# Kernel optimization log

Hardware: AMD Instinct MI355X
Metric: run time of the kernel (lower is better)

Reference implementation:

```python
import jax, jax.numpy as jnp
import numpy as np

VAR0, VAR1 = 0.1, 0.2          # SSD encode variances
POS_T, NEG_T, NPR = 0.5, 0.4, 3  # pos/neg thresholds, negpos_ratio
BBOX_ALPHA, CONF_ALPHA = 1.5, 1.0


def point_form(b):
    # cxcywh -> x1y1x2y2
    return jnp.concatenate([b[..., :2] - b[..., 2:] / 2, b[..., :2] + b[..., 2:] / 2], -1)


def jaccard(a, b):
    # a:[n,4], b:[m,4] in xyxy -> IoU [n,m]
    tl = jnp.maximum(a[:, None, :2], b[None, :, :2])
    br = jnp.minimum(a[:, None, 2:], b[None, :, 2:])
    inter = jnp.prod(jnp.clip(br - tl, 0.0), -1)
    area_a = jnp.prod(a[:, 2:] - a[:, :2], -1)[:, None]
    area_b = jnp.prod(b[:, 2:] - b[:, :2], -1)[None, :]
    return inter / jnp.clip(area_a + area_b - inter, 1e-10)


def encode(matched, priors):
    # matched: xyxy GT per prior; priors: cxcywh
    g_c = ((matched[:, :2] + matched[:, 2:]) / 2 - priors[:, :2]) / (VAR0 * priors[:, 2:])
    g_wh = jnp.log(jnp.clip((matched[:, 2:] - matched[:, :2]) / priors[:, 2:], 1e-8)) / VAR1
    return jnp.concatenate([g_c, g_wh], -1)


def match_one(gt_box, gt_lab, priors):
    # gt_box:[G,4] xyxy, gt_lab:[G], priors:[P,4] cxcywh
    ov = jaccard(gt_box, point_form(priors))            # [G,P]
    bt_over = ov.max(0)                                  # best GT overlap per prior [P]
    bt_idx = ov.argmax(0)                                # [P]
    bp_idx = ov.argmax(1)                                # best prior per GT [G]
    G = gt_box.shape[0]
    bt_over = bt_over.at[bp_idx].set(2.0)                # force-match best priors
    bt_idx = bt_idx.at[bp_idx].set(jnp.arange(G))
    matched = gt_box[bt_idx]                             # [P,4]
    conf_t = gt_lab[bt_idx]
    conf_t = jnp.where(bt_over < POS_T, jnp.where(bt_over < NEG_T, 0, -1), conf_t)
    return encode(matched, priors), conf_t


def reference(loc_data, conf_data, priors, gt_bboxes, gt_labels):
    B, P, C = conf_data.shape
    loc_t, conf_t = jax.vmap(match_one)(gt_bboxes, gt_labels, priors)
    loc_t = jax.lax.stop_gradient(loc_t)                 # targets are detached in torch
    pos = conf_t > 0                                     # [B,P]
    num_pos = pos.sum(-1)                                # [B]
    dt = loc_data.dtype
    pos_w = pos.astype(dt) / jnp.clip(num_pos, 1).astype(dt)[:, None]

    # localization: per-image-normalized smooth L1 over positives
    d = loc_data - loc_t
    sl1 = jnp.where(jnp.abs(d) < 1.0, 0.5 * d * d, jnp.abs(d) - 0.5)
    loss_B = (pos_w[:, :, None] * sl1).sum() * BBOX_ALPHA

    # OHEM confidence loss: mine top negpos_ratio*num_pos hardest negatives per image
    loss_c = jax.nn.logsumexp(conf_data, -1) - conf_data[..., 0]
    loss_c = jnp.where(pos | (conf_t < 0), 0.0, jax.lax.stop_gradient(loss_c))
    rank = jnp.argsort(jnp.argsort(-loss_c, -1), -1)     # descending rank [B,P]
    num_neg = jnp.clip(NPR * num_pos, 0, P - 1)
    neg = (rank < num_neg[:, None]) & (conf_t == 0)
    keep = (pos | neg).astype(dt)
    logp = jax.nn.log_softmax(conf_data, -1)
    tgt = jnp.clip(conf_t, 0)
    ce = -jnp.take_along_axis(logp, tgt[..., None], -1)[..., 0]
    loss_C = (keep * ce).sum() * CONF_ALPHA

    return jnp.stack([loss_B, loss_C]) / B               # [2]: (loss_B, loss_C)


def setup_inputs() -> dict:
    key = jax.random.key(0)
    k = jax.random.split(key, 8)
    B, P, C, G = 16, 19248, 81, 16
    loc_data = jax.random.normal(k[0], (B, P, 4), jnp.float32)
    conf_data = jax.random.normal(k[1], (B, P, C), jnp.float32)
    pc = jax.random.uniform(k[2], (B, P, 2)) * 0.9 + 0.05
    pwh = jax.random.uniform(k[3], (B, P, 2)) * 0.25 + 0.05
    priors = jnp.concatenate([pc, pwh], -1).astype(jnp.float32)  # cxcywh
    gc = jax.random.uniform(k[4], (B, G, 2)) * 0.8 + 0.1
    gwh = jax.random.uniform(k[5], (B, G, 2)) * 0.3 + 0.05
    gt_bboxes = jnp.clip(point_form(jnp.concatenate([gc, gwh], -1)), 0.0, 1.0).astype(jnp.float32)
    gt_labels = jax.random.randint(k[6], (B, G), 1, C)
    return {"loc_data": loc_data, "conf_data": conf_data, "priors": priors,
            "gt_bboxes": gt_bboxes, "gt_labels": gt_labels}
```

## Files before the change

### kernel.cpp

```cpp
#include <hip/hip_runtime.h>
#include <math.h>

#define NB 16
#define NP 19248
#define NC 81
#define NG 16
#define NBM 76
#define NBC 301
#define NWPB (NBC * 4)

static __device__ __forceinline__ float smoothl1(float d) {
    float a = fabsf(d);
    return (a < 1.f) ? 0.5f * d * d : (a - 0.5f);
}

static __device__ __forceinline__ unsigned long long umax64(unsigned long long a, unsigned long long b) {
    return a > b ? a : b;
}

__global__ void k_init(unsigned int* w, float* out) {
    if (threadIdx.x < 512) w[threadIdx.x] = 0u;
    if (threadIdx.x < 2) out[threadIdx.x] = 0.f;
}

__global__ void k_match(const float* __restrict__ priors,
                        const float* __restrict__ gtb,
                        unsigned long long* __restrict__ bp_key) {
    const int b = blockIdx.y;
    const int p = blockIdx.x * 256 + threadIdx.x;
    const bool valid = p < NP;
    __shared__ float4 sgt[NG];
    __shared__ unsigned long long smax[NG];
    if (threadIdx.x < NG) {
        const float* g4 = gtb + (size_t)(b * NG + threadIdx.x) * 4;
        sgt[threadIdx.x] = make_float4(g4[0], g4[1], g4[2], g4[3]);
        smax[threadIdx.x] = 0ULL;
    }
    __syncthreads();
    float4 pr = make_float4(0.f, 0.f, 0.f, 0.f);
    if (valid) pr = *(const float4*)(priors + ((size_t)b * NP + p) * 4);
    const float px1 = pr.x - pr.z * 0.5f, py1 = pr.y - pr.w * 0.5f;
    const float px2 = pr.x + pr.z * 0.5f, py2 = pr.y + pr.w * 0.5f;
    const float areaP = (px2 - px1) * (py2 - py1);
    const unsigned int pk = 0xFFFFFFFFu - (unsigned int)p;
    #pragma unroll
    for (int g = 0; g < NG; ++g) {
        float4 gb = sgt[g];
        float iw = fminf(gb.z, px2) - fmaxf(gb.x, px1);
        float ih = fminf(gb.w, py2) - fmaxf(gb.y, py1);
        float inter = fmaxf(iw, 0.f) * fmaxf(ih, 0.f);
        float areaG = (gb.z - gb.x) * (gb.w - gb.y);
        float ov = inter / fmaxf(areaG + areaP - inter, 1e-10f);
        unsigned long long key = ((unsigned long long)__float_as_uint(ov) << 32) | pk;
        #pragma unroll
        for (int off = 1; off <= 8; off <<= 1)
            key = umax64(key, (unsigned long long)__shfl_xor((unsigned long long)key, off));
        if ((threadIdx.x & 15) == 0) atomicMax(&smax[g], key);
    }
    __syncthreads();
    if (threadIdx.x < NG) atomicMax(&bp_key[b * NG + threadIdx.x], smax[threadIdx.x]);
}

__global__ void __launch_bounds__(256, 6) k_conf(
        const float* __restrict__ conf,
        const float* __restrict__ loc,
        const float* __restrict__ priors,
        const float* __restrict__ gtb,
        const int* __restrict__ gtl,
        const unsigned long long* __restrict__ bp_key,
        float* __restrict__ mlc,
        int* __restrict__ pnp, float* __restrict__ psl, float* __restrict__ pce) {
    __shared__ float sc[4][1296];
    const int b = blockIdx.y;
    const int tid = threadIdx.x;
    const int w = tid >> 6, lane = tid & 63;
    const int rb = blockIdx.x * 64 + w * 16;
    const bool wvalid = rb < NP;
    const int rb_c = wvalid ? rb : (NP - 16);

    const float4* src = (const float4*)(conf + ((size_t)b * NP + rb_c) * 81);
    float4* dst = (float4*)sc[w];
    #pragma unroll
    for (int i = 0; i < 5; ++i) dst[lane + 64 * i] = src[lane + 64 * i];
    if (lane < 4) dst[lane + 320] = src[lane + 320];

    const int r = lane >> 2, c = lane & 3;
    const int p = rb_c + r;
    const int bp = b * NP + p;

    const float4 prr = *(const float4*)(priors + (size_t)bp * 4);
    const float px1 = prr.x - prr.z * 0.5f, py1 = prr.y - prr.w * 0.5f;
    const float px2 = prr.x + prr.z * 0.5f, py2 = prr.y + prr.w * 0.5f;
    const float areaP = (px2 - px1) * (py2 - py1);
    unsigned long long kq = 0ULL;
    #pragma unroll
    for (int j = 0; j < 4; ++j) {
        const int g = c * 4 + j;
        const float* g4 = gtb + (size_t)(b * NG + g) * 4;
        float gx1 = g4[0], gy1 = g4[1], gx2 = g4[2], gy2 = g4[3];
        float iw = fminf(gx2, px2) - fmaxf(gx1, px1);
        float ih = fminf(gy2, py2) - fmaxf(gy1, py1);
        float inter = fmaxf(iw, 0.f) * fmaxf(ih, 0.f);
        float areaG = (gx2 - gx1) * (gy2 - gy1);
        float ov = inter / fmaxf(areaG + areaP - inter, 1e-10f);
        kq = umax64(kq, ((unsigned long long)__float_as_uint(ov) << 32) |
                        (unsigned long long)(15 - g));
    }
    kq = umax64(kq, (unsigned long long)__shfl_xor((unsigned long long)kq, 1, 4));
    kq = umax64(kq, (unsigned long long)__shfl_xor((unsigned long long)kq, 2, 4));
    const float over = __uint_as_float((unsigned int)(kq >> 32));
    int bi = 15 - (int)(kq & 0xFULL);

    int ct;
    if (over < 0.4f) ct = 0;
    else if (over < 0.5f) ct = -1;
    else ct = gtl[b * NG + bi];
    #pragma unroll
    for (int g = NG - 1; g >= 0; --g) {
        unsigned int fp = 0xFFFFFFFFu - (unsigned int)(bp_key[b * NG + g] & 0xFFFFFFFFULL);
        if (fp == (unsigned int)p) { bi = g; ct = gtl[b * NG + g]; break; }
    }
    if (!wvalid) ct = 0;
    const int tgt = ct > 0 ? ct : 0;

    __builtin_amdgcn_wave_barrier();

    const float* row = sc[w] + r * 81;
    float s = 0.f, ctg = 0.f;
    #pragma unroll
    for (int k = 0; k < 21; ++k) {
        int cc = c + 4 * k;
        if (cc < 81) {
            float v = row[cc];
            s += __expf(v);
            ctg += (cc == tgt) ? v : 0.f;
        }
    }
    s += __shfl_xor(s, 1, 4);   s += __shfl_xor(s, 2, 4);
    ctg += __shfl_xor(ctg, 1, 4); ctg += __shfl_xor(ctg, 2, 4);
    const float c0 = row[0];
    const float lse = __logf(s);

    if (c == 0 && wvalid) mlc[bp] = (ct == 0) ? (lse - c0) : -1.0f;

    float vsl = 0.f, vce = 0.f; int vnp = 0;
    if (c == 0 && ct > 0) {
        const float* gb = gtb + (size_t)(b * NG + bi) * 4;
        float lt0 = ((gb[0] + gb[2]) * 0.5f - prr.x) / (0.1f * prr.z);
        float lt1 = ((gb[1] + gb[3]) * 0.5f - prr.y) / (0.1f * prr.w);
        float lt2 = logf(fmaxf((gb[2] - gb[0]) / prr.z, 1e-8f)) / 0.2f;
        float lt3 = logf(fmaxf((gb[3] - gb[1]) / prr.w, 1e-8f)) / 0.2f;
        const float4 l4 = *(const float4*)(loc + (size_t)bp * 4);
        vsl = smoothl1(l4.x - lt0) + smoothl1(l4.y - lt1) +
              smoothl1(l4.z - lt2) + smoothl1(l4.w - lt3);
        vce = lse - ctg;
        vnp = 1;
    }
    #pragma unroll
    for (int o = 32; o >= 1; o >>= 1) {
        vnp += __shfl_xor(vnp, o);
        vsl += __shfl_xor(vsl, o);
        vce += __shfl_xor(vce, o);
    }
    if (lane == 0) {
        const int idx = b * NWPB + blockIdx.x * 4 + w;
        pnp[idx] = vnp; psl[idx] = vsl; pce[idx] = vce;
    }
}

__global__ void __launch_bounds__(1024) k_selneg(
        const float* __restrict__ mlc,
        const int* __restrict__ pnp,
        const float* __restrict__ psl,
        const float* __restrict__ pce,
        float* __restrict__ out) {
    const int b = blockIdx.x, tid = threadIdx.x;
    __shared__ unsigned int hist[4096];
    __shared__ unsigned long long list[1024];
    __shared__ unsigned int s_jstar, s_need, s_cnt;
    __shared__ unsigned long long s_thr;
    __shared__ unsigned int wtot[16], wsuf[16];
    __shared__ float wsum[16];
    __shared__ int wnp[16]; __shared__ float wsl[16], wcp[16];
    __shared__ int s_np; __shared__ float s_sl, s_cp;

    const float4* v4 = (const float4*)(mlc + (size_t)b * NP);
    float4 rv[5];
    #pragma unroll
    for (int j = 0; j < 5; ++j) {
        int i = tid + 1024 * j;
        rv[j] = (i < NP / 4) ? v4[i] : make_float4(-1.f, -1.f, -1.f, -1.f);
    }

    {
        int np_ = 0; float sl_ = 0.f, cp_ = 0.f;
        for (int i = tid; i < NWPB; i += 1024) {
            np_ += pnp[b * NWPB + i];
            sl_ += psl[b * NWPB + i];
            cp_ += pce[b * NWPB + i];
        }
        #pragma unroll
        for (int o = 32; o >= 1; o >>= 1) {
            np_ += __shfl_xor(np_, o);
            sl_ += __shfl_xor(sl_, o);
            cp_ += __shfl_xor(cp_, o);
        }
        if ((tid & 63) == 0) { wnp[tid >> 6] = np_; wsl[tid >> 6] = sl_; wcp[tid >> 6] = cp_; }
    }
    if (tid == 0) { s_cnt = 0u; s_thr = ~0ULL; }
    for (int i = tid; i < 4096; i += 1024) hist[i] = 0u;
    __syncthreads();
    if (tid == 0) {
        int np_ = 0; float sl_ = 0.f, cp_ = 0.f;
        #pragma unroll
        for (int i = 0; i < 16; ++i) { np_ += wnp[i]; sl_ += wsl[i]; cp_ += wcp[i]; }
        s_np = np_; s_sl = sl_; s_cp = cp_;
    }
    #pragma unroll
    for (int j = 0; j < 5; ++j) {
        float vv[4] = {rv[j].x, rv[j].y, rv[j].z, rv[j].w};
        #pragma unroll
        for (int c = 0; c < 4; ++c)
            if (vv[c] >= 0.f)
                atomicAdd(&hist[min((unsigned int)(vv[c] * 256.f), 4095u)], 1u);
    }
    __syncthreads();
    const int np = s_np;
    const unsigned int k = (unsigned int)min(3 * np, NP - 1);

    if (k > 0) {
        unsigned int c0 = hist[tid * 4], c1 = hist[tid * 4 + 1],
                     c2 = hist[tid * 4 + 2], c3 = hist[tid * 4 + 3];
        unsigned int t2 = c2 + c3, t1 = c1 + t2, t0 = c0 + t1;
        unsigned int s = t0;
        const int lane = tid & 63, w = tid >> 6;
        #pragma unroll
        for (int o = 1; o < 64; o <<= 1) {
            unsigned int vv = __shfl_down(s, o);
            if (lane + o < 64) s += vv;
        }
        if (lane == 0) wtot[w] = s;
        __syncthreads();
        if (tid < 16) {
            unsigned int acc = 0;
            for (int j = tid + 1; j < 16; ++j) acc += wtot[j];
            wsuf[tid] = acc;
        }
        __syncthreads();
        const unsigned int base = wsuf[w] + (s - t0);
        unsigned int b0 = base + t0, b1 = base + t1, b2 = base + t2, b3 = base + c3;
        hist[tid * 4] = b0; hist[tid * 4 + 1] = b1;
        hist[tid * 4 + 2] = b2; hist[tid * 4 + 3] = b3;
        __syncthreads();
        const unsigned int total = hist[0];
        if (k >= total) {
            if (tid == 0) s_thr = 0ULL;
        } else {
            unsigned int n3 = (tid * 4 + 4 < 4096) ? hist[tid * 4 + 4] : 0u;
            if (b0 >= k && b1 < k) { s_jstar = tid * 4;     s_need = k - b1; }
            if (b1 >= k && b2 < k) { s_jstar = tid * 4 + 1; s_need = k - b2; }
            if (b2 >= k && b3 < k) { s_jstar = tid * 4 + 2; s_need = k - b3; }
            if (b3 >= k && n3 < k) { s_jstar = tid * 4 + 3; s_need = k - n3; }
            __syncthreads();
            const unsigned int jstar = s_jstar, need = s_need;
            #pragma unroll
            for (int j = 0; j < 5; ++j) {
                float vv[4] = {rv[j].x, rv[j].y, rv[j].z, rv[j].w};
                #pragma unroll
                for (int c = 0; c < 4; ++c) {
                    if (vv[c] >= 0.f &&
                        min((unsigned int)(vv[c] * 256.f), 4095u) == jstar) {
                        unsigned int pos = atomicAdd(&s_cnt, 1u);
                        if (pos < 1024u) {
                            int pidx = 4 * (tid + 1024 * j) + c;
                            list[pos] = ((unsigned long long)__float_as_uint(vv[c]) << 32) |
                                        (unsigned long long)(0xFFFFFFFFu - (unsigned int)pidx);
                        }
                    }
                }
            }
            __syncthreads();
            const unsigned int cnt = s_cnt;
            if (cnt <= 1024u) {
                if (tid < (int)cnt) {
                    unsigned long long me = list[tid];
                    unsigned int rk = 0;
                    for (unsigned int j = 0; j < cnt; ++j) rk += (list[j] > me) ? 1u : 0u;
                    if (rk == need - 1) s_thr = me;
                }
            } else if (tid == 0) {
                s_thr = ((unsigned long long)__float_as_uint((float)jstar / 256.f)) << 32;
            }
        }
    }
    __syncthreads();
    const unsigned long long thr = s_thr;

    float sum = 0.f;
    #pragma unroll
    for (int j = 0; j < 5; ++j) {
        float vv[4] = {rv[j].x, rv[j].y, rv[j].z, rv[j].w};
        #pragma unroll
        for (int c = 0; c < 4; ++c) {
            if (vv[c] >= 0.f) {
                int pidx = 4 * (tid + 1024 * j) + c;
                unsigned long long key = ((unsigned long long)__float_as_uint(vv[c]) << 32) |
                                         (unsigned long long)(0xFFFFFFFFu - (unsigned int)pidx);
                if (key >= thr) sum += vv[c];
            }
        }
    }
    #pragma unroll
    for (int o = 32; o >= 1; o >>= 1) sum += __shfl_xor(sum, o);
    if ((tid & 63) == 0) wsum[tid >> 6] = sum;
    __syncthreads();
    if (tid == 0) {
        float neg = 0.f;
        #pragma unroll
        for (int i = 0; i < 16; ++i) neg += wsum[i];
        float lb = s_sl / (float)max(np, 1);
        float lc = s_cp + neg;
        atomicAdd(&out[0], lb * 1.5f / (float)NB);
        atomicAdd(&out[1], lc / (float)NB);
    }
}

extern "C" void kernel_launch(void* const* d_in, const int* in_sizes, int n_in,
                              void* d_out, int out_size, void* d_ws, size_t ws_size,
                              hipStream_t stream) {
    const float* loc    = (const float*)d_in[0];
    const float* conf   = (const float*)d_in[1];
    const float* priors = (const float*)d_in[2];
    const float* gtb    = (const float*)d_in[3];
    const int*   gtl    = (const int*)d_in[4];
    float* out = (float*)d_out;

    char* w = (char*)d_ws;
    const size_t P1 = (size_t)NB * NWPB * 4;
    unsigned long long* bp_key = (unsigned long long*)w;
    int*   pnp = (int*)  (w + 4096);
    float* psl = (float*)(w + 4096 + P1);
    float* pce = (float*)(w + 4096 + 2 * P1);
    float* mlc = (float*)(w + 262144);

    k_init<<<1, 512, 0, stream>>>((unsigned int*)w, out);
    k_match<<<dim3(NBM, NB), 256, 0, stream>>>(priors, gtb, bp_key);
    k_conf<<<dim3(NBC, NB), 256, 0, stream>>>(conf, loc, priors, gtb, gtl,
                                              bp_key, mlc, pnp, psl, pce);
    k_selneg<<<NB, 1024, 0, stream>>>(mlc, pnp, psl, pce, out);
}
```

Before: 185.9 us.

## Fuse prior matching into conf kernel and apply force-match corrections in finish

Removes the separate init and match kernels. The main conf kernel now also writes per-wave best-prior-per-GT keys to a workspace. The finish kernel reduces those keys, recomputes the force-matched priors, and applies delta corrections to the positive count, box loss, CE and the negative-mining candidates. This cuts two launches and a full extra pass over the priors, at the cost of a larger workspace and a more intricate correction path in the final kernel.

```diff
diff --git a/kernel.cpp b/kernel.cpp
--- a/kernel.cpp
+++ b/kernel.cpp
@@ -5,7 +5,6 @@
 #define NP 19248
 #define NC 81
 #define NG 16
-#define NBM 76
 #define NBC 301
 #define NWPB (NBC * 4)
 
@@ -18,108 +17,69 @@
     return a > b ? a : b;
 }
 
-__global__ void k_init(unsigned int* w, float* out) {
-    if (threadIdx.x < 512) w[threadIdx.x] = 0u;
-    if (threadIdx.x < 2) out[threadIdx.x] = 0.f;
-}
-
-__global__ void k_match(const float* __restrict__ priors,
-                        const float* __restrict__ gtb,
-                        unsigned long long* __restrict__ bp_key) {
+__global__ void __launch_bounds__(256, 6) k_main(
+        const float* __restrict__ conf,
+        const float* __restrict__ loc,
+        const float* __restrict__ priors,
+        const float* __restrict__ gtb,
+        const int* __restrict__ gtl,
+        unsigned long long* __restrict__ kws,
+        float* __restrict__ mlc,
+        int* __restrict__ pnp, float* __restrict__ psl, float* __restrict__ pce,
+        float* __restrict__ out) {
+    __shared__ float sc[4][1296];
     const int b = blockIdx.y;
-    const int p = blockIdx.x * 256 + threadIdx.x;
-    const bool valid = p < NP;
-    __shared__ float4 sgt[NG];
-    __shared__ unsigned long long smax[NG];
-    if (threadIdx.x < NG) {
-        const float* g4 = gtb + (size_t)(b * NG + threadIdx.x) * 4;
-        sgt[threadIdx.x] = make_float4(g4[0], g4[1], g4[2], g4[3]);
-        smax[threadIdx.x] = 0ULL;
-    }
-    __syncthreads();
-    float4 pr = make_float4(0.f, 0.f, 0.f, 0.f);
-    if (valid) pr = *(const float4*)(priors + ((size_t)b * NP + p) * 4);
-    const float px1 = pr.x - pr.z * 0.5f, py1 = pr.y - pr.w * 0.5f;
-    const float px2 = pr.x + pr.z * 0.5f, py2 = pr.y + pr.w * 0.5f;
+    const int tid = threadIdx.x;
+    if (b == 0 && blockIdx.x == 0 && tid < 2) out[tid] = 0.f;
+    const int w = tid >> 6, lane = tid & 63;
+    const int rb = blockIdx.x * 64 + w * 16;
+    const bool wvalid = rb < NP;
+    const int rb_c = wvalid ? rb : (NP - 16);
+
+    const float4* src = (const float4*)(conf + ((size_t)b * NP + rb_c) * 81);
+    float4* dst = (float4*)sc[w];
+    #pragma unroll
+    for (int i = 0; i < 5; ++i) dst[lane + 64 * i] = src[lane + 64 * i];
+    if (lane < 4) dst[lane + 320] = src[lane + 320];
+
+    const int r = lane >> 2, c = lane & 3;
+    const int p = rb_c + r;
+    const int bp = b * NP + p;
+    const int wslot = blockIdx.x * 4 + w;
+
+    const float4 prr = *(const float4*)(priors + (size_t)bp * 4);
+    const float px1 = prr.x - prr.z * 0.5f, py1 = prr.y - prr.w * 0.5f;
+    const float px2 = prr.x + prr.z * 0.5f, py2 = prr.y + prr.w * 0.5f;
     const float areaP = (px2 - px1) * (py2 - py1);
     const unsigned int pk = 0xFFFFFFFFu - (unsigned int)p;
-    #pragma unroll
-    for (int g = 0; g < NG; ++g) {
-        float4 gb = sgt[g];
+    unsigned long long kq = 0ULL;
+    #pragma unroll
+    for (int j = 0; j < 4; ++j) {
+        const int g = c * 4 + j;
+        const float4 gb = *(const float4*)(gtb + (size_t)(b * NG + g) * 4);
         float iw = fminf(gb.z, px2) - fmaxf(gb.x, px1);
         float ih = fminf(gb.w, py2) - fmaxf(gb.y, py1);
         float inter = fmaxf(iw, 0.f) * fmaxf(ih, 0.f);
         float areaG = (gb.z - gb.x) * (gb.w - gb.y);
         float ov = inter / fmaxf(areaG + areaP - inter, 1e-10f);
-        unsigned long long key = ((unsigned long long)__float_as_uint(ov) << 32) | pk;
-        #pragma unroll
-        for (int off = 1; off <= 8; off <<= 1)
-            key = umax64(key, (unsigned long long)__shfl_xor((unsigned long long)key, off));
-        if ((threadIdx.x & 15) == 0) atomicMax(&smax[g], key);
-    }
-    __syncthreads();
-    if (threadIdx.x < NG) atomicMax(&bp_key[b * NG + threadIdx.x], smax[threadIdx.x]);
-}
-
-__global__ void __launch_bounds__(256, 6) k_conf(
-        const float* __restrict__ conf,
-        const float* __restrict__ loc,
-        const float* __restrict__ priors,
-        const float* __restrict__ gtb,
-        const int* __restrict__ gtl,
-        const unsigned long long* __restrict__ bp_key,
-        float* __restrict__ mlc,
-        int* __restrict__ pnp, float* __restrict__ psl, float* __restrict__ pce) {
-    __shared__ float sc[4][1296];
-    const int b = blockIdx.y;
-    const int tid = threadIdx.x;
-    const int w = tid >> 6, lane = tid & 63;
-    const int rb = blockIdx.x * 64 + w * 16;
-    const bool wvalid = rb < NP;
-    const int rb_c = wvalid ? rb : (NP - 16);
-
-    const float4* src = (const float4*)(conf + ((size_t)b * NP + rb_c) * 81);
-    float4* dst = (float4*)sc[w];
-    #pragma unroll
-    for (int i = 0; i < 5; ++i) dst[lane + 64 * i] = src[lane + 64 * i];
-    if (lane < 4) dst[lane + 320] = src[lane + 320];
-
-    const int r = lane >> 2, c = lane & 3;
-    const int p = rb_c + r;
-    const int bp = b * NP + p;
-
-    const float4 prr = *(const float4*)(priors + (size_t)bp * 4);
-    const float px1 = prr.x - prr.z * 0.5f, py1 = prr.y - prr.w * 0.5f;
-    const float px2 = prr.x + prr.z * 0.5f, py2 = prr.y + prr.w * 0.5f;
-    const float areaP = (px2 - px1) * (py2 - py1);
-    unsigned long long kq = 0ULL;
-    #pragma unroll
-    for (int j = 0; j < 4; ++j) {
-        const int g = c * 4 + j;
-        const float* g4 = gtb + (size_t)(b * NG + g) * 4;
-        float gx1 = g4[0], gy1 = g4[1], gx2 = g4[2], gy2 = g4[3];
-        float iw = fminf(gx2, px2) - fmaxf(gx1, px1);
-        float ih = fminf(gy2, py2) - fmaxf(gy1, py1);
-        float inter = fmaxf(iw, 0.f) * fmaxf(ih, 0.f);
-        float areaG = (gx2 - gx1) * (gy2 - gy1);
-        float ov = inter / fmaxf(areaG + areaP - inter, 1e-10f);
-        kq = umax64(kq, ((unsigned long long)__float_as_uint(ov) << 32) |
-                        (unsigned long long)(15 - g));
+        const unsigned long long ub = (unsigned long long)__float_as_uint(ov) << 32;
+        kq = umax64(kq, ub | (unsigned long long)(15 - g));
+        unsigned long long kg = ub | (unsigned long long)pk;
+        #pragma unroll
+        for (int off = 4; off <= 32; off <<= 1)
+            kg = umax64(kg, (unsigned long long)__shfl_xor((unsigned long long)kg, off));
+        if (lane < 4)
+            kws[((size_t)(b * NG) + lane * 4 + j) * NWPB + wslot] = kg;
     }
     kq = umax64(kq, (unsigned long long)__shfl_xor((unsigned long long)kq, 1, 4));
     kq = umax64(kq, (unsigned long long)__shfl_xor((unsigned long long)kq, 2, 4));
     const float over = __uint_as_float((unsigned int)(kq >> 32));
-    int bi = 15 - (int)(kq & 0xFULL);
+    const int bi = 15 - (int)(kq & 0xFULL);
 
     int ct;
     if (over < 0.4f) ct = 0;
     else if (over < 0.5f) ct = -1;
     else ct = gtl[b * NG + bi];
-    #pragma unroll
-    for (int g = NG - 1; g >= 0; --g) {
-        unsigned int fp = 0xFFFFFFFFu - (unsigned int)(bp_key[b * NG + g] & 0xFFFFFFFFULL);
-        if (fp == (unsigned int)p) { bi = g; ct = gtl[b * NG + g]; break; }
-    }
     if (!wvalid) ct = 0;
     const int tgt = ct > 0 ? ct : 0;
 
@@ -145,11 +105,11 @@
 
     float vsl = 0.f, vce = 0.f; int vnp = 0;
     if (c == 0 && ct > 0) {
-        const float* gb = gtb + (size_t)(b * NG + bi) * 4;
-        float lt0 = ((gb[0] + gb[2]) * 0.5f - prr.x) / (0.1f * prr.z);
-        float lt1 = ((gb[1] + gb[3]) * 0.5f - prr.y) / (0.1f * prr.w);
-        float lt2 = logf(fmaxf((gb[2] - gb[0]) / prr.z, 1e-8f)) / 0.2f;
-        float lt3 = logf(fmaxf((gb[3] - gb[1]) / prr.w, 1e-8f)) / 0.2f;
+        const float4 gb = *(const float4*)(gtb + (size_t)(b * NG + bi) * 4);
+        float lt0 = ((gb.x + gb.z) * 0.5f - prr.x) / (0.1f * prr.z);
+        float lt1 = ((gb.y + gb.w) * 0.5f - prr.y) / (0.1f * prr.w);
+        float lt2 = logf(fmaxf((gb.z - gb.x) / prr.z, 1e-8f)) / 0.2f;
+        float lt3 = logf(fmaxf((gb.w - gb.y) / prr.w, 1e-8f)) / 0.2f;
         const float4 l4 = *(const float4*)(loc + (size_t)bp * 4);
         vsl = smoothl1(l4.x - lt0) + smoothl1(l4.y - lt1) +
               smoothl1(l4.z - lt2) + smoothl1(l4.w - lt3);
@@ -163,12 +123,18 @@
         vce += __shfl_xor(vce, o);
     }
     if (lane == 0) {
-        const int idx = b * NWPB + blockIdx.x * 4 + w;
+        const int idx = b * NWPB + wslot;
         pnp[idx] = vnp; psl[idx] = vsl; pce[idx] = vce;
     }
 }
 
-__global__ void __launch_bounds__(1024) k_selneg(
+__global__ void __launch_bounds__(1024) k_finish(
+        const float* __restrict__ conf,
+        const float* __restrict__ loc,
+        const float* __restrict__ priors,
+        const float* __restrict__ gtb,
+        const int* __restrict__ gtl,
+        const unsigned long long* __restrict__ kws,
         const float* __restrict__ mlc,
         const int* __restrict__ pnp,
         const float* __restrict__ psl,
@@ -183,6 +149,9 @@
     __shared__ float wsum[16];
     __shared__ int wnp[16]; __shared__ float wsl[16], wcp[16];
     __shared__ int s_np; __shared__ float s_sl, s_cp;
+    __shared__ unsigned int fprior[16];
+    __shared__ unsigned int zap[16];
+    __shared__ int s_dnp; __shared__ float s_dsl, s_dce;
 
     const float4* v4 = (const float4*)(mlc + (size_t)b * NP);
     float4 rv[5];
@@ -207,11 +176,118 @@
         }
         if ((tid & 63) == 0) { wnp[tid >> 6] = np_; wsl[tid >> 6] = sl_; wcp[tid >> 6] = cp_; }
     }
-    if (tid == 0) { s_cnt = 0u; s_thr = ~0ULL; }
+    {
+        const int wv = tid >> 6, lane = tid & 63;
+        unsigned long long kk = 0ULL;
+        const unsigned long long* kp = kws + ((size_t)(b * NG) + wv) * NWPB;
+        for (int i = lane; i < NWPB; i += 64) kk = umax64(kk, kp[i]);
+        #pragma unroll
+        for (int o = 32; o >= 1; o >>= 1)
+            kk = umax64(kk, (unsigned long long)__shfl_xor((unsigned long long)kk, o));
+        if (lane == 0) fprior[wv] = 0xFFFFFFFFu - (unsigned int)(kk & 0xFFFFFFFFULL);
+    }
+    if (tid == 0) { s_cnt = 0u; s_thr = ~0ULL; s_dnp = 0; s_dsl = 0.f; s_dce = 0.f; }
     for (int i = tid; i < 4096; i += 1024) hist[i] = 0u;
     __syncthreads();
+
+    if (tid < 64) {
+        const int g = tid >> 2, c = tid & 3;
+        const unsigned int pstar = fprior[g];
+        bool winner = true;
+        for (int g2 = g + 1; g2 < NG; ++g2) if (fprior[g2] == pstar) winner = false;
+        int old_ct = 1;
+        if (winner) {
+            const int pp = (int)pstar;
+            const int bpp = b * NP + pp;
+            const float4 prr = *(const float4*)(priors + (size_t)bpp * 4);
+            const float px1 = prr.x - prr.z * 0.5f, py1 = prr.y - prr.w * 0.5f;
+            const float px2 = prr.x + prr.z * 0.5f, py2 = prr.y + prr.w * 0.5f;
+            const float areaP = (px2 - px1) * (py2 - py1);
+            unsigned long long kq = 0ULL;
+            #pragma unroll
+            for (int j = 0; j < 4; ++j) {
+                const int g2 = c * 4 + j;
+                const float4 gb = *(const float4*)(gtb + (size_t)(b * NG + g2) * 4);
+                float iw = fminf(gb.z, px2) - fmaxf(gb.x, px1);
+                float ih = fminf(gb.w, py2) - fmaxf(gb.y, py1);
+                float inter = fmaxf(iw, 0.f) * fmaxf(ih, 0.f);
+                float areaG = (gb.z - gb.x) * (gb.w - gb.y);
+                float ov = inter / fmaxf(areaG + areaP - inter, 1e-10f);
+                kq = umax64(kq, ((unsigned long long)__float_as_uint(ov) << 32) |
+                                (unsigned long long)(15 - g2));
+            }
+            kq = umax64(kq, (unsigned long long)__shfl_xor((unsigned long long)kq, 1, 4));
+            kq = umax64(kq, (unsigned long long)__shfl_xor((unsigned long long)kq, 2, 4));
+            const float over = __uint_as_float((unsigned int)(kq >> 32));
+            const int obi = 15 - (int)(kq & 0xFULL);
+            if (over < 0.4f) old_ct = 0;
+            else if (over < 0.5f) old_ct = -1;
+            else old_ct = gtl[b * NG + obi];
+            const int new_lab = gtl[b * NG + g];
+            const int old_tgt = old_ct > 0 ? old_ct : 0;
+            const float* row = conf + (size_t)bpp * 81;
+            float s = 0.f, vnew = 0.f, vold = 0.f;
+            #pragma unroll
+            for (int k = 0; k < 21; ++k) {
+                int cc = c + 4 * k;
+                if (cc < 81) {
+                    float v = row[cc];
+                    s += __expf(v);
+                    vnew += (cc == new_lab) ? v : 0.f;
+                    vold += (cc == old_tgt) ? v : 0.f;
+                }
+            }
+            s += __shfl_xor(s, 1, 4);       s += __shfl_xor(s, 2, 4);
+            vnew += __shfl_xor(vnew, 1, 4); vnew += __shfl_xor(vnew, 2, 4);
+            vold += __shfl_xor(vold, 1, 4); vold += __shfl_xor(vold, 2, 4);
+            if (c == 0) {
+                const float lse = __logf(s);
+                float dce = (old_ct > 0) ? (vold - vnew) : (lse - vnew);
+                const float4 gb = *(const float4*)(gtb + (size_t)(b * NG + g) * 4);
+                float lt0 = ((gb.x + gb.z) * 0.5f - prr.x) / (0.1f * prr.z);
+                float lt1 = ((gb.y + gb.w) * 0.5f - prr.y) / (0.1f * prr.w);
+                float lt2 = logf(fmaxf((gb.z - gb.x) / prr.z, 1e-8f)) / 0.2f;
+                float lt3 = logf(fmaxf((gb.w - gb.y) / prr.w, 1e-8f)) / 0.2f;
+                const float4 l4 = *(const float4*)(loc + (size_t)bpp * 4);
+                float dsl = smoothl1(l4.x - lt0) + smoothl1(l4.y - lt1) +
+                            smoothl1(l4.z - lt2) + smoothl1(l4.w - lt3);
+                if (old_ct > 0) {
+                    const float4 go = *(const float4*)(gtb + (size_t)(b * NG + obi) * 4);
+                    float ot0 = ((go.x + go.z) * 0.5f - prr.x) / (0.1f * prr.z);
+                    float ot1 = ((go.y + go.w) * 0.5f - prr.y) / (0.1f * prr.w);
+                    float ot2 = logf(fmaxf((go.z - go.x) / prr.z, 1e-8f)) / 0.2f;
+                    float ot3 = logf(fmaxf((go.w - go.y) / prr.w, 1e-8f)) / 0.2f;
+                    dsl -= smoothl1(l4.x - ot0) + smoothl1(l4.y - ot1) +
+                           smoothl1(l4.z - ot2) + smoothl1(l4.w - ot3);
+                }
+                if (old_ct <= 0) atomicAdd(&s_dnp, 1);
+                atomicAdd(&s_dsl, dsl);
+                atomicAdd(&s_dce, dce);
+            }
+        }
+        if (c == 0) zap[g] = (winner && old_ct == 0) ? pstar : 0xFFFFFFFFu;
+    }
+    __syncthreads();
+
+    #pragma unroll
+    for (int z = 0; z < NG; ++z) {
+        unsigned int u = zap[z];
+        if (u != 0xFFFFFFFFu) {
+            unsigned int q = u >> 2, cc = u & 3u;
+            if ((int)(q & 1023u) == tid) {
+                unsigned int jj = q >> 10;
+                #pragma unroll
+                for (int j = 0; j < 5; ++j) if ((unsigned int)j == jj) {
+                    if (cc == 0) rv[j].x = -1.f;
+                    else if (cc == 1) rv[j].y = -1.f;
+                    else if (cc == 2) rv[j].z = -1.f;
+                    else rv[j].w = -1.f;
+                }
+            }
+        }
+    }
     if (tid == 0) {
-        int np_ = 0; float sl_ = 0.f, cp_ = 0.f;
+        int np_ = s_dnp; float sl_ = s_dsl, cp_ = s_dce;
         #pragma unroll
         for (int i = 0; i < 16; ++i) { np_ += wnp[i]; sl_ += wsl[i]; cp_ += wcp[i]; }
         s_np = np_; s_sl = sl_; s_cp = cp_;
@@ -220,9 +296,9 @@
     for (int j = 0; j < 5; ++j) {
         float vv[4] = {rv[j].x, rv[j].y, rv[j].z, rv[j].w};
         #pragma unroll
-        for (int c = 0; c < 4; ++c)
-            if (vv[c] >= 0.f)
-                atomicAdd(&hist[min((unsigned int)(vv[c] * 256.f), 4095u)], 1u);
+        for (int cth = 0; cth < 4; ++cth)
+            if (vv[cth] >= 0.f)
+                atomicAdd(&hist[min((unsigned int)(vv[cth] * 256.f), 4095u)], 1u);
     }
     __syncthreads();
     const int np = s_np;
@@ -267,13 +343,13 @@
             for (int j = 0; j < 5; ++j) {
                 float vv[4] = {rv[j].x, rv[j].y, rv[j].z, rv[j].w};
                 #pragma unroll
-                for (int c = 0; c < 4; ++c) {
-                    if (vv[c] >= 0.f &&
-                        min((unsigned int)(vv[c] * 256.f), 4095u) == jstar) {
+                for (int cth = 0; cth < 4; ++cth) {
+                    if (vv[cth] >= 0.f &&
+                        min((unsigned int)(vv[cth] * 256.f), 4095u) == jstar) {
                         unsigned int pos = atomicAdd(&s_cnt, 1u);
                         if (pos < 1024u) {
-                            int pidx = 4 * (tid + 1024 * j) + c;
-                            list[pos] = ((unsigned long long)__float_as_uint(vv[c]) << 32) |
+                            int pidx = 4 * (tid + 1024 * j) + cth;
+                            list[pos] = ((unsigned long long)__float_as_uint(vv[cth]) << 32) |
                                         (unsigned long long)(0xFFFFFFFFu - (unsigned int)pidx);
                         }
                     }
@@ -301,12 +377,12 @@
     for (int j = 0; j < 5; ++j) {
         float vv[4] = {rv[j].x, rv[j].y, rv[j].z, rv[j].w};
         #pragma unroll
-        for (int c = 0; c < 4; ++c) {
-            if (vv[c] >= 0.f) {
-                int pidx = 4 * (tid + 1024 * j) + c;
-                unsigned long long key = ((unsigned long long)__float_as_uint(vv[c]) << 32) |
+        for (int cth = 0; cth < 4; ++cth) {
+            if (vv[cth] >= 0.f) {
+                int pidx = 4 * (tid + 1024 * j) + cth;
+                unsigned long long key = ((unsigned long long)__float_as_uint(vv[cth]) << 32) |
                                          (unsigned long long)(0xFFFFFFFFu - (unsigned int)pidx);
-                if (key >= thr) sum += vv[c];
+                if (key >= thr) sum += vv[cth];
             }
         }
     }
@@ -336,16 +412,16 @@
     float* out = (float*)d_out;
 
     char* w = (char*)d_ws;
-    const size_t P1 = (size_t)NB * NWPB * 4;
-    unsigned long long* bp_key = (unsigned long long*)w;
-    int*   pnp = (int*)  (w + 4096);
-    float* psl = (float*)(w + 4096 + P1);
-    float* pce = (float*)(w + 4096 + 2 * P1);
-    float* mlc = (float*)(w + 262144);
-
-    k_init<<<1, 512, 0, stream>>>((unsigned int*)w, out);
-    k_match<<<dim3(NBM, NB), 256, 0, stream>>>(priors, gtb, bp_key);
-    k_conf<<<dim3(NBC, NB), 256, 0, stream>>>(conf, loc, priors, gtb, gtl,
-                                              bp_key, mlc, pnp, psl, pce);
-    k_selneg<<<NB, 1024, 0, stream>>>(mlc, pnp, psl, pce, out);
+    const size_t KWS = (size_t)NB * NG * NWPB * 8;
+    const size_t P1  = (size_t)NB * NWPB * 4;
+    unsigned long long* kws = (unsigned long long*)w;
+    int*   pnp = (int*)  (w + KWS);
+    float* psl = (float*)(w + KWS + P1);
+    float* pce = (float*)(w + KWS + 2 * P1);
+    float* mlc = (float*)(w + KWS + 3 * P1);
+
+    k_main<<<dim3(NBC, NB), 256, 0, stream>>>(conf, loc, priors, gtb, gtl,
+                                              kws, mlc, pnp, psl, pce, out);
+    k_finish<<<NB, 1024, 0, stream>>>(conf, loc, priors, gtb, gtl,
+                                      kws, mlc, pnp, psl, pce, out);
 }
```

New measurement: 186.1 us, median of 2. Within noise of the previous version (+0.1%).
